# Kernel tuning notes

Measured on AMD Instinct MI355X. Metric: run time of the kernel, lower is better.

Reference implementation:

```python
import jax, jax.numpy as jnp
import numpy as np

B, S, H, D = 2, 2048, 16, 64

def setup_inputs() -> dict:
    key = jax.random.key(0)
    kq, kk, kv = jax.random.split(key, 3)
    q = jax.random.normal(kq, (B, S, H, D), dtype=jnp.float32)
    k = jax.random.normal(kk, (B, S, H, D), dtype=jnp.float32)
    v = jax.random.normal(kv, (B, S, H, D), dtype=jnp.float32)
    return {"q": q, "k": k, "v": v}

def reference(q, k, v):
    # q, k, v: [B, S, H, D]; single-process path == full softmax attention,
    # which is exactly what the ring online-softmax computes over all chunks.
    d = q.shape[-1]
    scale = 1.0 / jnp.sqrt(jnp.asarray(d, dtype=q.dtype))
    # scores: [B, H, Sq, Sk]
    scores = jnp.einsum("bqhd,bkhd->bhqk", q, k) * scale
    attn = jax.nn.softmax(scores, axis=-1)
    # output back in [B, S, H, D] layout (torch transposes back)
    out = jnp.einsum("bhqk,bkhd->bqhd", attn, v)
    return out
```

## Files before the change

kernel.cpp:

```cpp
#include <hip/hip_runtime.h>
#include <hip/hip_bf16.h>

namespace {

constexpr int Sseq = 2048;
constexpr int NH   = 16;
constexpr int HD   = 64;
constexpr int ROW  = NH * HD;
constexpr int BN   = 64;
constexpr int NT   = Sseq / BN;
constexpr int BMm  = 64;
constexpr size_t IMG_BYTES = 16384;
constexpr size_t WS_NEED   = (size_t)32 * NT * IMG_BYTES;
constexpr float QSCALE = 0.18033688011112042f;

typedef __bf16 bf16_t;
typedef __attribute__((ext_vector_type(8))) bf16_t bf16x8;
typedef __attribute__((ext_vector_type(4))) float f32x4;
typedef __attribute__((ext_vector_type(2))) unsigned int u32x2;
typedef __attribute__((ext_vector_type(4))) unsigned int u32x4;

union Frag { bf16x8 v; unsigned int u[4]; };

__device__ inline unsigned int pkbf(float a, float b) {
  union { __hip_bfloat162 h; unsigned int u; } x;
  x.h = __float22bfloat162_rn(make_float2(a, b));
  return x.u;
}

__device__ inline void dma16(const void* g, void* l) {
  __builtin_amdgcn_global_load_lds(
      (const __attribute__((address_space(1))) void*)g,
      (__attribute__((address_space(3))) void*)l, 16, 0, 0);
}


__global__ __launch_bounds__(256)
void prep_kv(const float* __restrict__ K, const float* __restrict__ V,
             unsigned short* __restrict__ ws) {
  const int id  = blockIdx.x;
  const int bh  = id & 31;
  const int t   = id >> 5;
  const int tid = threadIdx.x;

  const size_t base = (size_t)(bh >> 4) * Sseq * ROW + (size_t)(bh & 15) * HD
                    + (size_t)(t * BN) * ROW;
  const float* kb = K + base;
  const float* vb = V + base;

  unsigned short* gK = (unsigned short*)((char*)ws + (size_t)(bh * NT + t) * IMG_BYTES);
  unsigned short* gV = gK + 4096;

  {
    const int kr = tid >> 2;
    const int kd = (tid & 3) * 16;
    const float* p = kb + (size_t)kr * ROW + kd;
    f32x4 x0 = *(const f32x4*)(p);
    f32x4 x1 = *(const f32x4*)(p + 4);
    f32x4 x2 = *(const f32x4*)(p + 8);
    f32x4 x3 = *(const f32x4*)(p + 12);
    int c0 = ((tid & 3) * 2) ^ (kr & 7);
    int c1 = ((tid & 3) * 2 + 1) ^ (kr & 7);
    u32x4 w0, w1;
    w0.x = pkbf(x0[0], x0[1]); w0.y = pkbf(x0[2], x0[3]);
    w0.z = pkbf(x1[0], x1[1]); w0.w = pkbf(x1[2], x1[3]);
    w1.x = pkbf(x2[0], x2[1]); w1.y = pkbf(x2[2], x2[3]);
    w1.z = pkbf(x3[0], x3[1]); w1.w = pkbf(x3[2], x3[3]);
    *(u32x4*)(gK + kr * 64 + c0 * 8) = w0;
    *(u32x4*)(gK + kr * 64 + c1 * 8) = w1;
  }
  {
    const int n4 = (tid & 15) * 4;
    const int d4 = (tid >> 4) * 4;
    const float* p = vb + (size_t)n4 * ROW + d4;
    f32x4 r0 = *(const f32x4*)(p);
    f32x4 r1 = *(const f32x4*)(p + ROW);
    f32x4 r2 = *(const f32x4*)(p + 2 * ROW);
    f32x4 r3 = *(const f32x4*)(p + 3 * ROW);
    #pragma unroll
    for (int i = 0; i < 4; ++i) {
      int d = d4 + i;
      int chunk = (n4 >> 3) ^ (d & 7);
      u32x2 val; val.x = pkbf(r0[i], r1[i]); val.y = pkbf(r2[i], r3[i]);
      *(u32x2*)(gV + d * 64 + chunk * 8 + (n4 & 7)) = val;
    }
  }
}

__global__ __launch_bounds__(256, 4)
void fa_main(const float* __restrict__ Q, const unsigned short* __restrict__ ws,
             float* __restrict__ O) {
  const int id   = blockIdx.x;
  const int bh   = id & 31;
  const int qblk = id >> 5;
  const int tid  = threadIdx.x;
  const int wave = tid >> 6;
  const int lane = tid & 63;
  const int qd   = lane >> 4;
  const int lm   = lane & 15;

  const size_t base = (size_t)(bh >> 4) * Sseq * ROW + (size_t)(bh & 15) * HD;
  const float* qb = Q + base;
  float*       ob = O + base;
  const char*  imgs = (const char*)ws + (size_t)bh * NT * IMG_BYTES;

  __shared__ __align__(16) unsigned short KV[2][8192];
  __shared__ __align__(16) unsigned short PB[4][16 * 64];

  const int qrow0 = qblk * BMm + wave * 16;

  Frag qf[2];
  {
    const float* qp = qb + (size_t)(qrow0 + lm) * ROW;
    for (int ks = 0; ks < 2; ++ks) {
      f32x4 a = *(const f32x4*)(qp + ks * 32 + qd * 8);
      f32x4 c = *(const f32x4*)(qp + ks * 32 + qd * 8 + 4);
      qf[ks].u[0] = pkbf(a[0] * QSCALE, a[1] * QSCALE);
      qf[ks].u[1] = pkbf(a[2] * QSCALE, a[3] * QSCALE);
      qf[ks].u[2] = pkbf(c[0] * QSCALE, c[1] * QSCALE);
      qf[ks].u[3] = pkbf(c[2] * QSCALE, c[3] * QSCALE);
    }
  }

  f32x4 oacc[4] = {};
  float lsum = 0.f;

  auto dma_tile = [&](int t, int b) {
    const char* img = imgs + (size_t)t * IMG_BYTES;
    char* dst = (char*)&KV[b][0];
    int woff = wave * 1024;
    #pragma unroll
    for (int j = 0; j < 4; ++j)
      dma16(img + j * 4096 + woff + lane * 16, dst + j * 4096 + woff);
  };

  dma_tile(0, 0);

  for (int t = 0; t < NT; ++t) {
    __syncthreads();
    if (t + 1 < NT) dma_tile(t + 1, (t + 1) & 1);

    const unsigned short* kt = &KV[t & 1][0];
    const unsigned short* vt = &KV[t & 1][4096];

    #pragma unroll
    for (int c = 0; c < 4; ++c) {
      Frag kf0, kf1;
      {
        int r = c * 16 + lm;
        int ch0 = (qd) ^ (lm & 7);
        int ch1 = (4 + qd) ^ (lm & 7);
        kf0.v = *(const bf16x8*)(kt + r * 64 + ch0 * 8);
        kf1.v = *(const bf16x8*)(kt + r * 64 + ch1 * 8);
      }
      f32x4 s = {};
      s = __builtin_amdgcn_mfma_f32_16x16x32_bf16(kf0.v, qf[0].v, s, 0, 0, 0);
      s = __builtin_amdgcn_mfma_f32_16x16x32_bf16(kf1.v, qf[1].v, s, 0, 0, 0);
      float e0 = __builtin_amdgcn_exp2f(s[0]);
      float e1 = __builtin_amdgcn_exp2f(s[1]);
      float e2 = __builtin_amdgcn_exp2f(s[2]);
      float e3 = __builtin_amdgcn_exp2f(s[3]);
      lsum += (e0 + e1) + (e2 + e3);
      int n = c * 16 + qd * 4;
      int chunk = (n >> 3) ^ (lm & 7);
      u32x2 val; val.x = pkbf(e0, e1); val.y = pkbf(e2, e3);
      *(u32x2*)(PB[wave] + lm * 64 + chunk * 8 + (n & 7)) = val;
    }

    __threadfence_block();

    #pragma unroll
    for (int ks = 0; ks < 2; ++ks) {
      bf16x8 pfr;
      {
        int chunk = (ks * 4 + qd) ^ (lm & 7);
        pfr = *(const bf16x8*)(PB[wave] + lm * 64 + chunk * 8);
      }
      #pragma unroll
      for (int dt = 0; dt < 4; ++dt) {
        int d = dt * 16 + lm;
        int chunk = (ks * 4 + qd) ^ (d & 7);
        bf16x8 vf = *(const bf16x8*)(vt + d * 64 + chunk * 8);
        oacc[dt] = __builtin_amdgcn_mfma_f32_16x16x32_bf16(vf, pfr, oacc[dt], 0, 0, 0);
      }
    }
  }

  {
    float l = lsum;
    l += __shfl_xor(l, 16, 64);
    l += __shfl_xor(l, 32, 64);
    float r = 1.0f / l;
    float* op = ob + (size_t)(qrow0 + lm) * ROW + qd * 4;
    #pragma unroll
    for (int dt = 0; dt < 4; ++dt) {
      f32x4 o = oacc[dt];
      o[0] *= r; o[1] *= r; o[2] *= r; o[3] *= r;
      *(f32x4*)(op + dt * 16) = o;
    }
  }
}

__global__ __launch_bounds__(256)
void fa_fwd_fb(const float* __restrict__ Q, const float* __restrict__ K,
               const float* __restrict__ V, float* __restrict__ O) {
  constexpr int BM = 128, MT = 2;
  const int id   = blockIdx.x;
  const int bh   = id & 31;
  const int qblk = id >> 5;
  const int tid  = threadIdx.x;
  const int wave = tid >> 6;
  const int lane = tid & 63;
  const int qd   = lane >> 4;
  const int lm   = lane & 15;

  const size_t base = (size_t)(bh >> 4) * Sseq * ROW + (size_t)(bh & 15) * HD;
  const float* qb = Q + base;
  const float* kb = K + base;
  const float* vb = V + base;
  float*       ob = O + base;

  __shared__ __align__(16) unsigned short KT[2][HD * 64];
  __shared__ __align__(16) unsigned short VT[2][HD * 64];
  __shared__ __align__(16) unsigned short PBf[4][MT][16 * 64];

  const int qrow0 = qblk * BM + wave * (MT * 16);

  Frag qf[MT][2];
  for (int mt = 0; mt < MT; ++mt) {
    const float* qp = qb + (size_t)(qrow0 + mt * 16 + lm) * ROW;
    for (int ks = 0; ks < 2; ++ks) {
      f32x4 a = *(const f32x4*)(qp + ks * 32 + qd * 8);
      f32x4 c = *(const f32x4*)(qp + ks * 32 + qd * 8 + 4);
      qf[mt][ks].u[0] = pkbf(a[0] * QSCALE, a[1] * QSCALE);
      qf[mt][ks].u[1] = pkbf(a[2] * QSCALE, a[3] * QSCALE);
      qf[mt][ks].u[2] = pkbf(c[0] * QSCALE, c[1] * QSCALE);
      qf[mt][ks].u[3] = pkbf(c[2] * QSCALE, c[3] * QSCALE);
    }
  }

  f32x4 oacc[MT][4] = {};
  float lsum[MT] = {};

  const int kr = tid >> 2;
  const int kd = (tid & 3) * 16;
  const int n4 = (tid & 15) * 4;
  const int d4 = (tid >> 4) * 4;

  const float* kp = kb + (size_t)kr * ROW + kd;
  const float* vp = vb + (size_t)n4 * ROW + d4;

  f32x4 kx0 = *(const f32x4*)(kp);
  f32x4 kx1 = *(const f32x4*)(kp + 4);
  f32x4 kx2 = *(const f32x4*)(kp + 8);
  f32x4 kx3 = *(const f32x4*)(kp + 12);
  f32x4 vx0 = *(const f32x4*)(vp);
  f32x4 vx1 = *(const f32x4*)(vp + ROW);
  f32x4 vx2 = *(const f32x4*)(vp + 2 * ROW);
  f32x4 vx3 = *(const f32x4*)(vp + 3 * ROW);

  for (int t = 0; t < NT; ++t) {
    unsigned short* kt = KT[t & 1];
    unsigned short* vt = VT[t & 1];

    {
      int c0 = ((tid & 3) * 2) ^ (kr & 7);
      int c1 = ((tid & 3) * 2 + 1) ^ (kr & 7);
      u32x4 w0, w1;
      w0.x = pkbf(kx0[0], kx0[1]); w0.y = pkbf(kx0[2], kx0[3]);
      w0.z = pkbf(kx1[0], kx1[1]); w0.w = pkbf(kx1[2], kx1[3]);
      w1.x = pkbf(kx2[0], kx2[1]); w1.y = pkbf(kx2[2], kx2[3]);
      w1.z = pkbf(kx3[0], kx3[1]); w1.w = pkbf(kx3[2], kx3[3]);
      *(u32x4*)(kt + kr * 64 + c0 * 8) = w0;
      *(u32x4*)(kt + kr * 64 + c1 * 8) = w1;
    }
    {
      #pragma unroll
      for (int i = 0; i < 4; ++i) {
        int d = d4 + i;
        int chunk = (n4 >> 3) ^ (d & 7);
        u32x2 val; val.x = pkbf(vx0[i], vx1[i]); val.y = pkbf(vx2[i], vx3[i]);
        *(u32x2*)(vt + d * 64 + chunk * 8 + (n4 & 7)) = val;
      }
    }

    __syncthreads();

    if (t + 1 < NT) {
      kp += BN * ROW; vp += BN * ROW;
      kx0 = *(const f32x4*)(kp);
      kx1 = *(const f32x4*)(kp + 4);
      kx2 = *(const f32x4*)(kp + 8);
      kx3 = *(const f32x4*)(kp + 12);
      vx0 = *(const f32x4*)(vp);
      vx1 = *(const f32x4*)(vp + ROW);
      vx2 = *(const f32x4*)(vp + 2 * ROW);
      vx3 = *(const f32x4*)(vp + 3 * ROW);
    }

    #pragma unroll
    for (int c = 0; c < 4; ++c) {
      Frag kf0, kf1;
      {
        int r = c * 16 + lm;
        int ch0 = (qd) ^ (lm & 7);
        int ch1 = (4 + qd) ^ (lm & 7);
        kf0.v = *(const bf16x8*)(kt + r * 64 + ch0 * 8);
        kf1.v = *(const bf16x8*)(kt + r * 64 + ch1 * 8);
      }
      #pragma unroll
      for (int mt = 0; mt < MT; ++mt) {
        f32x4 s = {};
        s = __builtin_amdgcn_mfma_f32_16x16x32_bf16(kf0.v, qf[mt][0].v, s, 0, 0, 0);
        s = __builtin_amdgcn_mfma_f32_16x16x32_bf16(kf1.v, qf[mt][1].v, s, 0, 0, 0);
        float e0 = __builtin_amdgcn_exp2f(s[0]);
        float e1 = __builtin_amdgcn_exp2f(s[1]);
        float e2 = __builtin_amdgcn_exp2f(s[2]);
        float e3 = __builtin_amdgcn_exp2f(s[3]);
        lsum[mt] += (e0 + e1) + (e2 + e3);
        int n = c * 16 + qd * 4;
        int chunk = (n >> 3) ^ (lm & 7);
        u32x2 val; val.x = pkbf(e0, e1); val.y = pkbf(e2, e3);
        *(u32x2*)(PBf[wave][mt] + lm * 64 + chunk * 8 + (n & 7)) = val;
      }
    }

    __threadfence_block();

    #pragma unroll
    for (int ks = 0; ks < 2; ++ks) {
      bf16x8 pfr[MT];
      #pragma unroll
      for (int mt = 0; mt < MT; ++mt) {
        int chunk = (ks * 4 + qd) ^ (lm & 7);
        pfr[mt] = *(const bf16x8*)(PBf[wave][mt] + lm * 64 + chunk * 8);
      }
      #pragma unroll
      for (int dt = 0; dt < 4; ++dt) {
        int d = dt * 16 + lm;
        int chunk = (ks * 4 + qd) ^ (d & 7);
        bf16x8 vf = *(const bf16x8*)(vt + d * 64 + chunk * 8);
        #pragma unroll
        for (int mt = 0; mt < MT; ++mt)
          oacc[mt][dt] = __builtin_amdgcn_mfma_f32_16x16x32_bf16(vf, pfr[mt], oacc[mt][dt], 0, 0, 0);
      }
    }
  }

  #pragma unroll
  for (int mt = 0; mt < MT; ++mt) {
    float l = lsum[mt];
    l += __shfl_xor(l, 16, 64);
    l += __shfl_xor(l, 32, 64);
    float r = 1.0f / l;
    float* op = ob + (size_t)(qrow0 + mt * 16 + lm) * ROW + qd * 4;
    #pragma unroll
    for (int dt = 0; dt < 4; ++dt) {
      f32x4 o = oacc[mt][dt];
      o[0] *= r; o[1] *= r; o[2] *= r; o[3] *= r;
      *(f32x4*)(op + dt * 16) = o;
    }
  }
}

}

extern "C" void kernel_launch(void* const* d_in, const int* in_sizes, int n_in,
                              void* d_out, int out_size, void* d_ws, size_t ws_size,
                              hipStream_t stream) {
  const float* q = (const float*)d_in[0];
  const float* k = (const float*)d_in[1];
  const float* v = (const float*)d_in[2];
  float* o = (float*)d_out;
  (void)in_sizes; (void)n_in; (void)out_size;
  if (ws_size >= WS_NEED) {
    hipLaunchKernelGGL(prep_kv, dim3(32 * NT), dim3(256), 0, stream,
                       k, v, (unsigned short*)d_ws);
    hipLaunchKernelGGL(fa_main, dim3(32 * (Sseq / BMm)), dim3(256), 0, stream,
                       q, (const unsigned short*)d_ws, o);
  } else {
    hipLaunchKernelGGL(fa_fwd_fb, dim3(2 * NH * (Sseq / 128)), dim3(256), 0, stream,
                       q, k, v, o);
  }
}
```

Baseline: 141.6 us.

## Use 32x32 MFMA with 128-row Q blocks and split-K across wave pairs

Replaces the 16x16x32 MFMA main kernel with 32x32x16 bf16 MFMAs. Each block now handles 128 query rows, and its four waves form two query groups × two key halves. Each wave keeps 64 query rows against half of each K/V tile, and the two halves' partial outputs and row sums are combined through shared memory at the end. The aim is more data reuse per LDS fragment load and fewer instructions per FLOP. The cost is higher register pressure (occupancy hint cut from 4 to 2 blocks per SM), half as many blocks, and an extra reduction pass through LDS.

```diff
diff --git a/kernel.cpp b/kernel.cpp
--- a/kernel.cpp
+++ b/kernel.cpp
@@ -9,7 +9,7 @@
 constexpr int ROW  = NH * HD;
 constexpr int BN   = 64;
 constexpr int NT   = Sseq / BN;
-constexpr int BMm  = 64;
+constexpr int BM   = 128;
 constexpr size_t IMG_BYTES = 16384;
 constexpr size_t WS_NEED   = (size_t)32 * NT * IMG_BYTES;
 constexpr float QSCALE = 0.18033688011112042f;
@@ -17,6 +17,7 @@
 typedef __bf16 bf16_t;
 typedef __attribute__((ext_vector_type(8))) bf16_t bf16x8;
 typedef __attribute__((ext_vector_type(4))) float f32x4;
+typedef __attribute__((ext_vector_type(16))) float f32x16;
 typedef __attribute__((ext_vector_type(2))) unsigned int u32x2;
 typedef __attribute__((ext_vector_type(4))) unsigned int u32x4;
 
@@ -87,7 +88,7 @@
   }
 }
 
-__global__ __launch_bounds__(256, 4)
+__global__ __launch_bounds__(256, 2)
 void fa_main(const float* __restrict__ Q, const unsigned short* __restrict__ ws,
              float* __restrict__ O) {
   const int id   = blockIdx.x;
@@ -96,34 +97,40 @@
   const int tid  = threadIdx.x;
   const int wave = tid >> 6;
   const int lane = tid & 63;
-  const int qd   = lane >> 4;
-  const int lm   = lane & 15;
+  const int wk   = wave & 1;
+  const int wq   = wave >> 1;
+  const int l31  = lane & 31;
+  const int h    = lane >> 5;
 
   const size_t base = (size_t)(bh >> 4) * Sseq * ROW + (size_t)(bh & 15) * HD;
   const float* qb = Q + base;
   float*       ob = O + base;
   const char*  imgs = (const char*)ws + (size_t)bh * NT * IMG_BYTES;
 
-  __shared__ __align__(16) unsigned short KV[2][8192];
-  __shared__ __align__(16) unsigned short PB[4][16 * 64];
-
-  const int qrow0 = qblk * BMm + wave * 16;
-
-  Frag qf[2];
-  {
-    const float* qp = qb + (size_t)(qrow0 + lm) * ROW;
-    for (int ks = 0; ks < 2; ++ks) {
-      f32x4 a = *(const f32x4*)(qp + ks * 32 + qd * 8);
-      f32x4 c = *(const f32x4*)(qp + ks * 32 + qd * 8 + 4);
-      qf[ks].u[0] = pkbf(a[0] * QSCALE, a[1] * QSCALE);
-      qf[ks].u[1] = pkbf(a[2] * QSCALE, a[3] * QSCALE);
-      qf[ks].u[2] = pkbf(c[0] * QSCALE, c[1] * QSCALE);
-      qf[ks].u[3] = pkbf(c[2] * QSCALE, c[3] * QSCALE);
-    }
-  }
-
-  f32x4 oacc[4] = {};
-  float lsum = 0.f;
+  __shared__ __align__(16) unsigned char smem[32768 + 20480 + 512];
+  unsigned short (*KV)[8192] = (unsigned short (*)[8192])smem;
+  unsigned char* pb  = smem + 32768 + wave * 5120;
+  float*         lsc = (float*)(smem + 32768 + 20480);
+
+  const int qrow0 = qblk * BM + wq * 64;
+
+  Frag qf[2][4];
+  #pragma unroll
+  for (int nt = 0; nt < 2; ++nt) {
+    const float* qp = qb + (size_t)(qrow0 + nt * 32 + l31) * ROW + h * 8;
+    #pragma unroll
+    for (int f = 0; f < 4; ++f) {
+      f32x4 a = *(const f32x4*)(qp + f * 16);
+      f32x4 b = *(const f32x4*)(qp + f * 16 + 4);
+      qf[nt][f].u[0] = pkbf(a[0] * QSCALE, a[1] * QSCALE);
+      qf[nt][f].u[1] = pkbf(a[2] * QSCALE, a[3] * QSCALE);
+      qf[nt][f].u[2] = pkbf(b[0] * QSCALE, b[1] * QSCALE);
+      qf[nt][f].u[3] = pkbf(b[2] * QSCALE, b[3] * QSCALE);
+    }
+  }
+
+  f32x16 oacc[2][2] = {};
+  float lsum[2] = {};
 
   auto dma_tile = [&](int t, int b) {
     const char* img = imgs + (size_t)t * IMG_BYTES;
@@ -143,60 +150,118 @@
     const unsigned short* kt = &KV[t & 1][0];
     const unsigned short* vt = &KV[t & 1][4096];
 
-    #pragma unroll
-    for (int c = 0; c < 4; ++c) {
-      Frag kf0, kf1;
-      {
-        int r = c * 16 + lm;
-        int ch0 = (qd) ^ (lm & 7);
-        int ch1 = (4 + qd) ^ (lm & 7);
-        kf0.v = *(const bf16x8*)(kt + r * 64 + ch0 * 8);
-        kf1.v = *(const bf16x8*)(kt + r * 64 + ch1 * 8);
-      }
-      f32x4 s = {};
-      s = __builtin_amdgcn_mfma_f32_16x16x32_bf16(kf0.v, qf[0].v, s, 0, 0, 0);
-      s = __builtin_amdgcn_mfma_f32_16x16x32_bf16(kf1.v, qf[1].v, s, 0, 0, 0);
-      float e0 = __builtin_amdgcn_exp2f(s[0]);
-      float e1 = __builtin_amdgcn_exp2f(s[1]);
-      float e2 = __builtin_amdgcn_exp2f(s[2]);
-      float e3 = __builtin_amdgcn_exp2f(s[3]);
-      lsum += (e0 + e1) + (e2 + e3);
-      int n = c * 16 + qd * 4;
-      int chunk = (n >> 3) ^ (lm & 7);
-      u32x2 val; val.x = pkbf(e0, e1); val.y = pkbf(e2, e3);
-      *(u32x2*)(PB[wave] + lm * 64 + chunk * 8 + (n & 7)) = val;
+    Frag ka[4];
+    {
+      int r = wk * 32 + l31;
+      const unsigned short* krow = kt + r * 64;
+      #pragma unroll
+      for (int f = 0; f < 4; ++f) {
+        int c = (2 * f + h) ^ (r & 7);
+        ka[f].v = *(const bf16x8*)(krow + c * 8);
+      }
+    }
+
+    #pragma unroll
+    for (int nt = 0; nt < 2; ++nt) {
+      f32x16 s = {};
+      #pragma unroll
+      for (int f = 0; f < 4; ++f)
+        s = __builtin_amdgcn_mfma_f32_32x32x16_bf16(ka[f].v, qf[nt][f].v, s, 0, 0, 0);
+      float e[16]; float ls = 0.f;
+      #pragma unroll
+      for (int i = 0; i < 16; ++i) { e[i] = __builtin_amdgcn_exp2f(s[i]); ls += e[i]; }
+      lsum[nt] += ls;
+      int qq = nt * 32 + l31;
+      unsigned char* prow = pb + qq * 80;
+      int sw = (qq >> 3) & 3;
+      #pragma unroll
+      for (int c2 = 0; c2 < 4; ++c2) {
+        u32x2 w;
+        w.x = pkbf(e[4 * c2],     e[4 * c2 + 1]);
+        w.y = pkbf(e[4 * c2 + 2], e[4 * c2 + 3]);
+        *(u32x2*)(prow + ((c2 ^ sw) * 16 + 8 * h)) = w;
+      }
     }
 
     __threadfence_block();
 
-    #pragma unroll
-    for (int ks = 0; ks < 2; ++ks) {
-      bf16x8 pfr;
-      {
-        int chunk = (ks * 4 + qd) ^ (lm & 7);
-        pfr = *(const bf16x8*)(PB[wave] + lm * 64 + chunk * 8);
-      }
-      #pragma unroll
-      for (int dt = 0; dt < 4; ++dt) {
-        int d = dt * 16 + lm;
-        int chunk = (ks * 4 + qd) ^ (d & 7);
-        bf16x8 vf = *(const bf16x8*)(vt + d * 64 + chunk * 8);
-        oacc[dt] = __builtin_amdgcn_mfma_f32_16x16x32_bf16(vf, pfr, oacc[dt], 0, 0, 0);
-      }
-    }
-  }
-
-  {
-    float l = lsum;
-    l += __shfl_xor(l, 16, 64);
-    l += __shfl_xor(l, 32, 64);
-    float r = 1.0f / l;
-    float* op = ob + (size_t)(qrow0 + lm) * ROW + qd * 4;
-    #pragma unroll
-    for (int dt = 0; dt < 4; ++dt) {
-      f32x4 o = oacc[dt];
-      o[0] *= r; o[1] *= r; o[2] *= r; o[3] *= r;
-      *(f32x4*)(op + dt * 16) = o;
+    Frag va[2][2];
+    #pragma unroll
+    for (int mt = 0; mt < 2; ++mt) {
+      int d = mt * 32 + l31;
+      const unsigned short* vrow = vt + d * 64;
+      #pragma unroll
+      for (int k2 = 0; k2 < 2; ++k2) {
+        int c = (4 * wk + 2 * k2 + h) ^ (d & 7);
+        va[mt][k2].v = *(const bf16x8*)(vrow + c * 8);
+      }
+    }
+
+    #pragma unroll
+    for (int nt = 0; nt < 2; ++nt) {
+      int qq = nt * 32 + l31;
+      const unsigned char* prow = pb + qq * 80;
+      int sw = (qq >> 3) & 3;
+      #pragma unroll
+      for (int k2 = 0; k2 < 2; ++k2) {
+        Frag pf;
+        pf.v = *(const bf16x8*)(prow + ((2 * k2 + h) ^ sw) * 16);
+        #pragma unroll
+        for (int mt = 0; mt < 2; ++mt)
+          oacc[mt][nt] = __builtin_amdgcn_mfma_f32_32x32x16_bf16(
+              va[mt][k2].v, pf.v, oacc[mt][nt], 0, 0, 0);
+      }
+    }
+  }
+
+  __syncthreads();
+  float* osc = (float*)smem;
+
+  #pragma unroll
+  for (int nt = 0; nt < 2; ++nt) lsum[nt] += __shfl_xor(lsum[nt], 32, 64);
+
+  if (wk == 1) {
+    if (h == 0) {
+      lsc[(wq * 2 + 0) * 32 + l31] = lsum[0];
+      lsc[(wq * 2 + 1) * 32 + l31] = lsum[1];
+    }
+    float* dst = osc + wq * 4096 + lane * 64;
+    #pragma unroll
+    for (int nt = 0; nt < 2; ++nt)
+      #pragma unroll
+      for (int mt = 0; mt < 2; ++mt)
+        #pragma unroll
+        for (int g = 0; g < 4; ++g) {
+          int idx = nt * 8 + mt * 4 + g;
+          f32x4 w;
+          w[0] = oacc[mt][nt][4 * g];     w[1] = oacc[mt][nt][4 * g + 1];
+          w[2] = oacc[mt][nt][4 * g + 2]; w[3] = oacc[mt][nt][4 * g + 3];
+          *(f32x4*)(dst + (idx ^ (lane & 15)) * 4) = w;
+        }
+  }
+  __syncthreads();
+  if (wk == 0) {
+    const float* src = osc + wq * 4096 + lane * 64;
+    #pragma unroll
+    for (int nt = 0; nt < 2; ++nt) {
+      float l = lsum[nt] + lsc[(wq * 2 + nt) * 32 + l31];
+      float r = 1.0f / l;
+      int q = qrow0 + nt * 32 + l31;
+      float* op = ob + (size_t)q * ROW;
+      #pragma unroll
+      for (int mt = 0; mt < 2; ++mt)
+        #pragma unroll
+        for (int g = 0; g < 4; ++g) {
+          int idx = nt * 8 + mt * 4 + g;
+          f32x4 w = *(const f32x4*)(src + (idx ^ (lane & 15)) * 4);
+          int dbase = mt * 32 + 8 * g + 4 * h;
+          f32x4 o;
+          o[0] = (oacc[mt][nt][4 * g]     + w[0]) * r;
+          o[1] = (oacc[mt][nt][4 * g + 1] + w[1]) * r;
+          o[2] = (oacc[mt][nt][4 * g + 2] + w[2]) * r;
+          o[3] = (oacc[mt][nt][4 * g + 3] + w[3]) * r;
+          *(f32x4*)(op + dbase) = o;
+        }
     }
   }
 }
@@ -204,7 +269,7 @@
 __global__ __launch_bounds__(256)
 void fa_fwd_fb(const float* __restrict__ Q, const float* __restrict__ K,
                const float* __restrict__ V, float* __restrict__ O) {
-  constexpr int BM = 128, MT = 2;
+  constexpr int BMf = 128, MT = 2;
   const int id   = blockIdx.x;
   const int bh   = id & 31;
   const int qblk = id >> 5;
@@ -224,7 +289,7 @@
   __shared__ __align__(16) unsigned short VT[2][HD * 64];
   __shared__ __align__(16) unsigned short PBf[4][MT][16 * 64];
 
-  const int qrow0 = qblk * BM + wave * (MT * 16);
+  const int qrow0 = qblk * BMf + wave * (MT * 16);
 
   Frag qf[MT][2];
   for (int mt = 0; mt < MT; ++mt) {
@@ -262,7 +327,6 @@
   for (int t = 0; t < NT; ++t) {
     unsigned short* kt = KT[t & 1];
     unsigned short* vt = VT[t & 1];
-
     {
       int c0 = ((tid & 3) * 2) ^ (kr & 7);
       int c1 = ((tid & 3) * 2 + 1) ^ (kr & 7);
@@ -283,9 +347,7 @@
         *(u32x2*)(vt + d * 64 + chunk * 8 + (n4 & 7)) = val;
       }
     }
-
     __syncthreads();
-
     if (t + 1 < NT) {
       kp += BN * ROW; vp += BN * ROW;
       kx0 = *(const f32x4*)(kp);
@@ -297,7 +359,6 @@
       vx2 = *(const f32x4*)(vp + 2 * ROW);
       vx3 = *(const f32x4*)(vp + 3 * ROW);
     }
-
     #pragma unroll
     for (int c = 0; c < 4; ++c) {
       Frag kf0, kf1;
@@ -324,9 +385,7 @@
         *(u32x2*)(PBf[wave][mt] + lm * 64 + chunk * 8 + (n & 7)) = val;
       }
     }
-
     __threadfence_block();
-
     #pragma unroll
     for (int ks = 0; ks < 2; ++ks) {
       bf16x8 pfr[MT];
@@ -376,7 +435,7 @@
   if (ws_size >= WS_NEED) {
     hipLaunchKernelGGL(prep_kv, dim3(32 * NT), dim3(256), 0, stream,
                        k, v, (unsigned short*)d_ws);
-    hipLaunchKernelGGL(fa_main, dim3(32 * (Sseq / BMm)), dim3(256), 0, stream,
+    hipLaunchKernelGGL(fa_main, dim3(32 * (Sseq / BM)), dim3(256), 0, stream,
                        q, (const unsigned short*)d_ws, o);
   } else {
     hipLaunchKernelGGL(fa_fwd_fb, dim3(2 * NH * (Sseq / 128)), dim3(256), 0, stream,
```

After: 141.1 us. About the same (-0.4%).
